# Optimization experiments

Hardware: AMD Instinct MI355X
Metric: run time of the kernel (lower is better)

Reference implementation:

```python
import jax, jax.numpy as jnp
import numpy as np

B, T, F = 4096, 60, 30
H, HD, LAT = 256, 100, 256
ACQ_VOCAB = [(50, 16), (10, 8), (5, 4)]
SEQ_VOCAB = [(30, 8), (12, 4), (31, 4)]
DIN = F + 28 + 16  # 74 = seq_n_features + emb_acq_sum + emb_seq_sum
EPS = 1e-5


def setup_inputs() -> dict:
    key = jax.random.key(0)
    ks = iter(jax.random.split(key, 64))

    def nrm(shape, s=0.05):
        return jax.random.normal(next(ks), shape, jnp.float32) * s

    inp = {}
    inp["seq"] = jax.random.normal(next(ks), (B, T, F), jnp.float32)
    inp["seq_len"] = jnp.sort(jax.random.randint(next(ks), (B,), 1, T + 1))[::-1]  # descending (pack_padded)
    inp["ymd"] = jnp.stack([jax.random.randint(next(ks), (B, T), 0, c) for c, _ in SEQ_VOCAB], axis=-1)
    inp["acq"] = jnp.stack([jax.random.randint(next(ks), (B,), 0, c) for c, _ in ACQ_VOCAB], axis=-1)
    inp["macro_pred"] = jax.random.normal(next(ks), (B, 12, 14), jnp.float32)
    inp["z_noise"] = jax.random.normal(next(ks), (B, LAT), jnp.float32)  # reparam noise, fixed for determinism
    for i, (c, d) in enumerate(ACQ_VOCAB):
        inp[f"E_acq{i}"] = nrm((c, d), 1.0)
    for i, (c, d) in enumerate(SEQ_VOCAB):
        inp[f"E_seq{i}"] = nrm((c, d), 1.0)
    for tag in ("f", "b"):  # bidirectional LSTM, 1 layer
        inp[f"Wih_{tag}"] = nrm((4 * H, DIN))
        inp[f"Whh_{tag}"] = nrm((4 * H, H))
        inp[f"bih_{tag}"] = nrm((4 * H,))
        inp[f"bhh_{tag}"] = nrm((4 * H,))
    inp["W_lat"] = nrm((2 * LAT, H)); inp["b_lat"] = nrm((2 * LAT,))
    inp["Wih1"] = nrm((4 * HD, LAT + 9 + 14)); inp["Whh1"] = nrm((4 * HD, HD))
    inp["bih1"] = nrm((4 * HD,)); inp["bhh1"] = nrm((4 * HD,))
    inp["Wih2"] = nrm((4 * HD, HD)); inp["Whh2"] = nrm((4 * HD, HD))
    inp["bih2"] = nrm((4 * HD,)); inp["bhh2"] = nrm((4 * HD,))
    inp["Wg1"] = nrm((25, HD)); inp["bg1"] = nrm((25,))
    inp["gamma"] = jnp.ones((25,), jnp.float32); inp["beta"] = jnp.zeros((25,), jnp.float32)
    inp["Wg2"] = nrm((9, 25)); inp["bg2"] = nrm((9,))
    return inp


def _lstm_cell(x, h, c, Wih, Whh, bih, bhh):
    g = x @ Wih.T + h @ Whh.T + (bih + bhh)
    i, f, gg, o = jnp.split(g, 4, axis=-1)  # torch gate order i,f,g,o
    c = jax.nn.sigmoid(f) * c + jax.nn.sigmoid(i) * jnp.tanh(gg)
    h = jax.nn.sigmoid(o) * jnp.tanh(c)
    return h, c


def _masked_lstm(xs_tm, lens, Wih, Whh, bih, bhh):
    """xs_tm: [T,B,D] time-major. Returns hidden at each sequence's final valid step."""
    h0 = jnp.zeros((xs_tm.shape[1], Whh.shape[1]), xs_tm.dtype)

    def step(carry, inp):
        h, c = carry
        x, t = inp
        hn, cn = _lstm_cell(x, h, c, Wih, Whh, bih, bhh)
        m = (t < lens)[:, None]
        return (jnp.where(m, hn, h), jnp.where(m, cn, c)), None

    (h, _), _ = jax.lax.scan(step, (h0, h0), (xs_tm, jnp.arange(xs_tm.shape[0])))
    return h


def reference(seq, seq_len, ymd, acq, macro_pred, z_noise,
              E_acq0, E_acq1, E_acq2, E_seq0, E_seq1, E_seq2,
              Wih_f, Whh_f, bih_f, bhh_f, Wih_b, Whh_b, bih_b, bhh_b,
              W_lat, b_lat, Wih1, Whh1, bih1, bhh1, Wih2, Whh2, bih2, bhh2,
              Wg1, bg1, gamma, beta, Wg2, bg2):
    Bn, Tn = seq.shape[0], seq.shape[1]
    ea = jnp.concatenate([E_acq0[acq[:, 0]], E_acq1[acq[:, 1]], E_acq2[acq[:, 2]]], axis=1)
    ea = jnp.broadcast_to(ea[:, None, :], (Bn, Tn, ea.shape[1]))
    ey = jnp.concatenate([E_seq0[ymd[:, :, 0]], E_seq1[ymd[:, :, 1]], E_seq2[ymd[:, :, 2]]], axis=2)
    s = jnp.concatenate([seq, ea, ey], axis=2)  # [B,T,74]

    # bidirectional LSTM over valid lengths (pack_padded semantics)
    h_f = _masked_lstm(jnp.swapaxes(s, 0, 1), seq_len, Wih_f, Whh_f, bih_f, bhh_f)
    idx = jnp.clip(seq_len[:, None] - 1 - jnp.arange(Tn)[None, :], 0, Tn - 1)  # per-seq reversed valid indices
    s_rev = jnp.take_along_axis(s, idx[:, :, None], axis=1)
    h_b = _masked_lstm(jnp.swapaxes(s_rev, 0, 1), seq_len, Wih_b, Whh_b, bih_b, bhh_b)

    lat = (h_f + h_b) @ W_lat.T + b_lat  # [B, 2*LAT]
    mu_z, logv = lat[:, :LAT], lat[:, LAT:]
    z = mu_z + jnp.sqrt(jnp.exp(logv)) * z_noise

    dlq0 = jnp.take_along_axis(seq, (seq_len - 1)[:, None, None], axis=1)[:, 0, -9:]  # [B,9]
    h0 = jnp.zeros((Bn, HD), seq.dtype)

    def dec_step(carry, mp_t):
        h1, c1, h2, c2, dlq = carry
        decinp = jnp.concatenate([z, dlq, mp_t], axis=1)  # [B, LAT+9+14]
        h1, c1 = _lstm_cell(decinp, h1, c1, Wih1, Whh1, bih1, bhh1)
        h2, c2 = _lstm_cell(h1, h2, c2, Wih2, Whh2, bih2, bhh2)  # dropout = identity (eval)
        x = jax.nn.relu(h2 @ Wg1.T + bg1)
        mu = x.mean(axis=0)
        var = ((x - mu) ** 2).mean(axis=0)  # train-mode BN, biased var
        x = gamma * (x - mu) * jax.lax.rsqrt(var + EPS) + beta
        dlq = x @ Wg2.T + bg2
        return (h1, c1, h2, c2, dlq), dlq

    _, outs = jax.lax.scan(dec_step, (h0, h0, h0, h0, dlq0), jnp.swapaxes(macro_pred, 0, 1))
    return jnp.transpose(outs, (1, 2, 0))  # [B, 9, 12] (torch.stack(out, 2))
```

## Files before the change

kernel.cpp:

```cpp
#include <hip/hip_runtime.h>
#include <math.h>

#define B_SZ   4096
#define T_SZ   60
#define F_SZ   30
#define H_ENC  256
#define HD_DEC 100
#define LATD   256
#define KM     352
#define KMP    360
#define NKK    11
#define DTAIL  24

enum {
  OFF_PWM_F = 0,
  OFF_PWM_B = OFF_PWM_F + 180224,
  OFF_BEN_F = OFF_PWM_B + 180224,
  OFF_BEN_B = OFF_BEN_F + 1024,
  OFF_PLAT  = OFF_BEN_B + 1024,
  OFF_P1I   = OFF_PLAT + 256*256*2,
  OFF_P1H   = OFF_P1I + 280*100*4,
  OFF_P2I   = OFF_P1H + 100*100*4,
  OFF_P2H   = OFF_P2I + 100*100*4,
  OFF_WG1T  = OFF_P2H + 100*100*4,
  OFF_BE1   = OFF_WG1T + 100*25,
  OFF_BE2   = OFF_BE1 + 400,
  OFF_HF    = OFF_BE2 + 400,
  OFF_HB    = OFF_HF + B_SZ*H_ENC,
  OFF_H1    = OFF_HB + B_SZ*H_ENC,
  OFF_C1    = OFF_H1 + B_SZ*HD_DEC,
  OFF_H2    = OFF_C1 + B_SZ*HD_DEC,
  OFF_C2    = OFF_H2 + B_SZ*HD_DEC,
  OFF_DLQ   = OFF_C2 + B_SZ*HD_DEC,
  OFF_XBUF  = OFF_DLQ + B_SZ*9,
  OFF_MU    = OFF_XBUF + B_SZ*25,
  OFF_RSTD  = OFF_MU + 25,
  OFF_ZW1   = OFF_RSTD + 25,
  WS_FLOATS = OFF_ZW1 + B_SZ*400
};

typedef __attribute__((ext_vector_type(8))) short short8v;
typedef __attribute__((ext_vector_type(4))) float f32x4;

__device__ __forceinline__ float sigf(float x) { return 1.0f / (1.0f + expf(-x)); }

__device__ __forceinline__ unsigned short f2bf(float f) {
  union { float f; unsigned int u; } v; v.f = f;
  unsigned int u = v.u + 0x7fffu + ((v.u >> 16) & 1u);
  return (unsigned short)(u >> 16);
}
__device__ __forceinline__ float bf2f(unsigned short s) {
  union { unsigned int u; float f; } v; v.u = ((unsigned int)s) << 16;
  return v.f;
}

struct PJob { const float* a; const float* b; float* dst; int p0, p1, p2, p3, mode; };
struct PrepArgs { PJob j[12]; };

__device__ __forceinline__ float enc_wv(const float* wih, const float* whh, int k, int u, int g) {
  if (k < 74)  return wih[(g * 256 + u) * 74 + k];
  if (k < 76)  return 0.0f;
  if (k < 332) return whh[(g * 256 + u) * 256 + (k - 76)];
  return 0.0f;
}

__global__ __launch_bounds__(256) void prep_kernel(PrepArgs pa) {
  int gtid = blockIdx.x * blockDim.x + threadIdx.x;
  int stride = gridDim.x * blockDim.x;
  for (int jj = 0; jj < 12; ++jj) {
    PJob jb = pa.j[jj];
    if (jb.mode == 1) {
      for (int i = gtid; i < jb.p0; i += stride) jb.dst[i] = jb.a[i] + jb.b[i];
    } else if (jb.mode == 0) {
      int total = jb.p2 * jb.p0;
      for (int i = gtid; i < total; i += stride) {
        int k = i / jb.p0, u = i - k * jb.p0;
        float* d = jb.dst + (size_t)i * jb.p3;
        for (int g = 0; g < jb.p3; ++g)
          d[g] = (k < jb.p1) ? jb.a[(g * jb.p0 + u) * jb.p1 + k] : 0.0f;
      }
    } else if (jb.mode == 4) {
      int total = NKK * 64 * 64;
      for (int i = gtid; i < total; i += stride) {
        int kk = i / 4096, rem = i - kk * 4096;
        int ntg = rem >> 6, l = rem & 63;
        int n = ntg * 16 + (l & 15);
        int u = n >> 2, g = n & 3;
        int kb = kk * 32 + (l >> 4) * 8;
        unsigned int* d = (unsigned int*)jb.dst + (size_t)i * 4;
        for (int wd = 0; wd < 4; ++wd) {
          float lo = enc_wv(jb.a, jb.b, kb + 2 * wd,     u, g);
          float hi = enc_wv(jb.a, jb.b, kb + 2 * wd + 1, u, g);
          d[wd] = (unsigned int)f2bf(lo) | ((unsigned int)f2bf(hi) << 16);
        }
      }
    } else {
      for (int i = gtid; i < 1024; i += stride) {
        int u = i >> 2, g = i & 3;
        jb.dst[i] = jb.a[g * 256 + u] + jb.b[g * 256 + u];
      }
    }
  }
}

#define GDOT(acc, c, w0, w1, w2, w3, xv) \
  acc = fmaf((w0).c, (xv).x, fmaf((w1).c, (xv).y, fmaf((w2).c, (xv).z, fmaf((w3).c, (xv).w, acc))))

__global__ __launch_bounds__(512) void enc_kernel(
    const float* __restrict__ seq, const int* __restrict__ seq_len,
    const int* __restrict__ ymd, const int* __restrict__ acq,
    const float* __restrict__ Ea0, const float* __restrict__ Ea1, const float* __restrict__ Ea2,
    const float* __restrict__ Es0, const float* __restrict__ Es1, const float* __restrict__ Es2,
    const unsigned short* __restrict__ PWMf, const unsigned short* __restrict__ PWMb,
    const float* __restrict__ benF, const float* __restrict__ benB,
    float* __restrict__ hf_out, float* __restrict__ hb_out)
{
  const int tid = threadIdx.x;
  const bool bwd = blockIdx.x >= 128;
  const int c = blockIdx.x & 127;
  const unsigned short* __restrict__ PWM = bwd ? PWMb : PWMf;
  const float* __restrict__ ben = bwd ? benB : benF;
  float* __restrict__ hout = bwd ? hb_out : hf_out;

  __shared__ __align__(16) unsigned short v_s[32][KMP];
  __shared__ float c_s[32][256];
  __shared__ int   len_s[32];

  for (int i = tid; i < 32 * KMP; i += 512) (&v_s[0][0])[i] = 0;
  for (int i = tid; i < 32 * 256; i += 512) (&c_s[0][0])[i] = 0.0f;
  if (tid < 32) len_s[tid] = seq_len[c + 128 * tid];
  __syncthreads();

  for (int i = tid; i < 32 * 28; i += 512) {
    int r = i / 28, d = i - r * 28;
    const int* aq = &acq[(c + 128 * r) * 3];
    float v;
    if (d < 16)      v = Ea0[aq[0] * 16 + d];
    else if (d < 24) v = Ea1[aq[1] * 8 + (d - 16)];
    else             v = Ea2[aq[2] * 4 + (d - 24)];
    v_s[r][30 + d] = f2bf(v);
  }

  const int w   = tid >> 6;
  const int l   = tid & 63;
  const int col = l & 15;
  const int qk  = l >> 4;
  const int g   = l & 3;
  const int usub = col >> 2;

  float bias_r[8];
  #pragma unroll
  for (int nt = 0; nt < 8; ++nt) bias_r[nt] = ben[128 * w + 16 * nt + col];

  __syncthreads();
  const int maxlen = len_s[0];

  for (int t = 0; t < maxlen; ++t) {
    for (int i = tid; i < 1472; i += 512) {
      if (i < 960) {
        int r = i / 30, k = i - r * 30;
        int len = len_s[r];
        int te = bwd ? max(len - 1 - t, 0) : t;
        v_s[r][k] = f2bf(seq[((size_t)(c + 128 * r) * T_SZ + te) * F_SZ + k]);
      } else {
        int ii = i - 960;
        int r = ii >> 4, d = ii & 15;
        int len = len_s[r];
        int te = bwd ? max(len - 1 - t, 0) : t;
        const int* ym = &ymd[((size_t)(c + 128 * r) * T_SZ + te) * 3];
        float v;
        if (d < 8)       v = Es0[ym[0] * 8 + d];
        else if (d < 12) v = Es1[ym[1] * 4 + (d - 8)];
        else             v = Es2[ym[2] * 4 + (d - 12)];
        v_s[r][58 + d] = f2bf(v);
      }
    }
    __syncthreads();

    f32x4 acc0[8], acc1[8];
    #pragma unroll
    for (int nt = 0; nt < 8; ++nt) {
      acc0[nt][0] = bias_r[nt]; acc0[nt][1] = bias_r[nt];
      acc0[nt][2] = bias_r[nt]; acc0[nt][3] = bias_r[nt];
      acc1[nt] = acc0[nt];
    }

    for (int kk = 0; kk < NKK; ++kk) {
      short8v a0 = *reinterpret_cast<const short8v*>(&v_s[col][32 * kk + 8 * qk]);
      short8v a1 = *reinterpret_cast<const short8v*>(&v_s[16 + col][32 * kk + 8 * qk]);
      const unsigned short* Bk = PWM + ((size_t)kk * 4096 + l) * 8;
      #pragma unroll
      for (int nt = 0; nt < 8; ++nt) {
        int ntg = 8 * w + nt;
        short8v b = *reinterpret_cast<const short8v*>(Bk + (size_t)ntg * 512);
        acc0[nt] = __builtin_amdgcn_mfma_f32_16x16x32_bf16(a0, b, acc0[nt], 0, 0, 0);
        acc1[nt] = __builtin_amdgcn_mfma_f32_16x16x32_bf16(a1, b, acc1[nt], 0, 0, 0);
      }
    }
    __syncthreads();

    #pragma unroll
    for (int rt = 0; rt < 2; ++rt) {
      #pragma unroll
      for (int nt = 0; nt < 8; ++nt) {
        int u = 32 * w + 4 * nt + usub;
        #pragma unroll
        for (int i = 0; i < 4; ++i) {
          int row = 16 * rt + qk * 4 + i;
          float val = rt == 0 ? acc0[nt][i] : acc1[nt][i];
          float act = (g == 2) ? tanhf(val) : sigf(val);
          float a1s = __shfl_xor(act, 1);
          float a2s = __shfl_xor(act, 2);
          float a3s = __shfl_xor(a1s, 2);
          if (g == 0 && t < len_s[row]) {
            float cc = c_s[row][u];
            float cn = a1s * cc + act * a2s;
            c_s[row][u] = cn;
            v_s[row][76 + u] = f2bf(a3s * tanhf(cn));
          }
        }
      }
    }
  }

  __syncthreads();
  for (int i = tid; i < 32 * 256; i += 512) {
    int r = i >> 8, u = i & 255;
    hout[(size_t)(c + 128 * r) * H_ENC + u] = bf2f(v_s[r][76 + u]);
  }
}

__global__ __launch_bounds__(256) void latent_kernel(
    const float* __restrict__ hf, const float* __restrict__ hb,
    const float2* __restrict__ Plat, const float* __restrict__ b_lat,
    const float* __restrict__ z_noise, const float* __restrict__ seq,
    const int* __restrict__ seq_len, const float4* __restrict__ P1I,
    float* __restrict__ dlq, float* __restrict__ zw1,
    float* __restrict__ h1w, float* __restrict__ c1w,
    float* __restrict__ h2w, float* __restrict__ c2w)
{
  const int tid = threadIdx.x;
  const int b0 = blockIdx.x * 16;
  __shared__ float hs[16][H_ENC];
  for (int i = tid; i < 16 * H_ENC; i += 256)
    (&hs[0][0])[i] = hf[b0 * H_ENC + i] + hb[b0 * H_ENC + i];
  __syncthreads();

  const int u = tid;
  const float bm = b_lat[u], bv = b_lat[LATD + u];
  float am[16], av[16];
  #pragma unroll
  for (int r = 0; r < 16; ++r) { am[r] = bm; av[r] = bv; }

  for (int k = 0; k < H_ENC; k += 4) {
    const float2 p0 = Plat[(k + 0) * 256 + u];
    const float2 p1 = Plat[(k + 1) * 256 + u];
    const float2 p2 = Plat[(k + 2) * 256 + u];
    const float2 p3 = Plat[(k + 3) * 256 + u];
    #pragma unroll
    for (int r = 0; r < 16; ++r) {
      const float4 hv = *reinterpret_cast<const float4*>(&hs[r][k]);
      am[r] = fmaf(p0.x, hv.x, fmaf(p1.x, hv.y, fmaf(p2.x, hv.z, fmaf(p3.x, hv.w, am[r]))));
      av[r] = fmaf(p0.y, hv.x, fmaf(p1.y, hv.y, fmaf(p2.y, hv.z, fmaf(p3.y, hv.w, av[r]))));
    }
  }
  if (u < HD_DEC) {
    #pragma unroll
    for (int r = 0; r < 16; ++r) {
      int b = b0 + r;
      h1w[b * HD_DEC + u] = 0.0f; c1w[b * HD_DEC + u] = 0.0f;
      h2w[b * HD_DEC + u] = 0.0f; c2w[b * HD_DEC + u] = 0.0f;
    }
  }
  if (u < 9) {
    #pragma unroll
    for (int r = 0; r < 16; ++r) {
      int b = b0 + r;
      int len = seq_len[b];
      dlq[b * 9 + u] = seq[(b * T_SZ + (len - 1)) * F_SZ + 21 + u];
    }
  }
  __syncthreads();
  #pragma unroll
  for (int r = 0; r < 16; ++r) {
    int b = b0 + r;
    hs[r][u] = am[r] + sqrtf(expf(av[r])) * z_noise[b * LATD + u];
  }
  __syncthreads();

  const int uu = tid & 127;
  const int grp = tid >> 7;
  const int r0 = grp * 8;
  if (uu < HD_DEC) {
    float a0[8], a1[8], a2[8], a3[8];
    #pragma unroll
    for (int r = 0; r < 8; ++r) { a0[r] = 0.0f; a1[r] = 0.0f; a2[r] = 0.0f; a3[r] = 0.0f; }
    for (int k = 0; k < LATD; k += 4) {
      const float4 w0 = P1I[(k + 0) * 100 + uu];
      const float4 w1 = P1I[(k + 1) * 100 + uu];
      const float4 w2 = P1I[(k + 2) * 100 + uu];
      const float4 w3 = P1I[(k + 3) * 100 + uu];
      #pragma unroll
      for (int r = 0; r < 8; ++r) {
        const float4 xv = *reinterpret_cast<const float4*>(&hs[r0 + r][k]);
        GDOT(a0[r], x, w0, w1, w2, w3, xv);
        GDOT(a1[r], y, w0, w1, w2, w3, xv);
        GDOT(a2[r], z, w0, w1, w2, w3, xv);
        GDOT(a3[r], w, w0, w1, w2, w3, xv);
      }
    }
    #pragma unroll
    for (int r = 0; r < 8; ++r) {
      int b = b0 + r0 + r;
      zw1[b * 400 + uu]       = a0[r];
      zw1[b * 400 + 100 + uu] = a1[r];
      zw1[b * 400 + 200 + uu] = a2[r];
      zw1[b * 400 + 300 + uu] = a3[r];
    }
  }
}

__global__ __launch_bounds__(256) void dec_cell_kernel(
    const float* __restrict__ zw1, const float* __restrict__ dlq0,
    const float* __restrict__ macro,
    float* __restrict__ h1w, float* __restrict__ c1w,
    float* __restrict__ h2w, float* __restrict__ c2w,
    const float4* __restrict__ P1I, const float4* __restrict__ P1H, const float* __restrict__ be1,
    const float4* __restrict__ P2I, const float4* __restrict__ P2H, const float* __restrict__ be2,
    const float* __restrict__ Wg1T, const float* __restrict__ bg1,
    const float* __restrict__ muv, const float* __restrict__ rstdv,
    const float* __restrict__ gamma, const float* __restrict__ beta,
    const float* __restrict__ Wg2, const float* __restrict__ bg2,
    float* __restrict__ xbuf, float* __restrict__ out, int t)
{
  const int tid = threadIdx.x;
  const int b0 = blockIdx.x * 16;
  __shared__ float di[16][DTAIL];
  __shared__ float xns[16][25];
  __shared__ float h1s[16][HD_DEC];
  __shared__ float h2s[16][HD_DEC];

  if (t > 0) {
    for (int p = tid; p < 16 * 25; p += 256) {
      int r = p / 25, cc = p - r * 25;
      xns[r][cc] = gamma[cc] * (xbuf[(b0 + r) * 25 + cc] - muv[cc]) * rstdv[cc] + beta[cc];
    }
  } else {
    for (int p = tid; p < 16 * 9; p += 256) {
      int r = p / 9, j = p - r * 9;
      di[r][j] = dlq0[(b0 + r) * 9 + j];
    }
  }
  for (int i = tid; i < 16 * 15; i += 256) {
    int r = i / 15, k = i - r * 15;
    di[r][9 + k] = (k < 14) ? macro[((size_t)(b0 + r) * 12 + t) * 14 + k] : 0.0f;
  }
  for (int i = tid; i < 16 * HD_DEC; i += 256) {
    int r = i / HD_DEC, k = i - r * HD_DEC;
    h1s[r][k] = h1w[(b0 + r) * HD_DEC + k];
    h2s[r][k] = h2w[(b0 + r) * HD_DEC + k];
  }
  __syncthreads();
  if (t > 0) {
    for (int p = tid; p < 16 * 9; p += 256) {
      int r = p / 9, j = p - r * 9;
      float s = bg2[j];
      #pragma unroll
      for (int cc = 0; cc < 25; ++cc) s += xns[r][cc] * Wg2[j * 25 + cc];
      di[r][j] = s;
      out[(size_t)(b0 + r) * 108 + j * 12 + (t - 1)] = s;
    }
  }

  const int u = tid & 127;
  const int grp = tid >> 7;
  const int r0 = grp * 8;
  const bool act = u < HD_DEC;

  float c1r[8], c2r[8];
  if (act) {
    #pragma unroll
    for (int r = 0; r < 8; ++r) {
      c1r[r] = c1w[(b0 + r0 + r) * HD_DEC + u];
      c2r[r] = c2w[(b0 + r0 + r) * HD_DEC + u];
    }
  }
  __syncthreads();

  float a0[8], a1[8], a2[8], a3[8];
  if (act) {
    const float b0g = be1[u], b1g = be1[100 + u], b2g = be1[200 + u], b3g = be1[300 + u];
    #pragma unroll
    for (int r = 0; r < 8; ++r) {
      const float* zw = &zw1[(size_t)(b0 + r0 + r) * 400];
      a0[r] = b0g + zw[u];
      a1[r] = b1g + zw[100 + u];
      a2[r] = b2g + zw[200 + u];
      a3[r] = b3g + zw[300 + u];
    }
    for (int k = 0; k < DTAIL; k += 4) {
      const int kk = LATD + k;
      const float4 w0 = P1I[(kk + 0) * 100 + u];
      const float4 w1 = P1I[(kk + 1) * 100 + u];
      const float4 w2 = P1I[(kk + 2) * 100 + u];
      const float4 w3 = P1I[(kk + 3) * 100 + u];
      #pragma unroll
      for (int r = 0; r < 8; ++r) {
        const float4 xv = *reinterpret_cast<const float4*>(&di[r0 + r][k]);
        GDOT(a0[r], x, w0, w1, w2, w3, xv);
        GDOT(a1[r], y, w0, w1, w2, w3, xv);
        GDOT(a2[r], z, w0, w1, w2, w3, xv);
        GDOT(a3[r], w, w0, w1, w2, w3, xv);
      }
    }
    for (int k = 0; k < HD_DEC; k += 4) {
      const float4 w0 = P1H[(k + 0) * 100 + u];
      const float4 w1 = P1H[(k + 1) * 100 + u];
      const float4 w2 = P1H[(k + 2) * 100 + u];
      const float4 w3 = P1H[(k + 3) * 100 + u];
      #pragma unroll
      for (int r = 0; r < 8; ++r) {
        const float4 hv = *reinterpret_cast<const float4*>(&h1s[r0 + r][k]);
        GDOT(a0[r], x, w0, w1, w2, w3, hv);
        GDOT(a1[r], y, w0, w1, w2, w3, hv);
        GDOT(a2[r], z, w0, w1, w2, w3, hv);
        GDOT(a3[r], w, w0, w1, w2, w3, hv);
      }
    }
  }
  __syncthreads();
  if (act) {
    #pragma unroll
    for (int r = 0; r < 8; ++r) {
      float ig = sigf(a0[r]), fg = sigf(a1[r]), gg = tanhf(a2[r]), og = sigf(a3[r]);
      float cn = fg * c1r[r] + ig * gg;
      float hn = og * tanhf(cn);
      int b = b0 + r0 + r;
      h1s[r0 + r][u] = hn;
      h1w[b * HD_DEC + u] = hn;
      c1w[b * HD_DEC + u] = cn;
    }
  }
  __syncthreads();

  if (act) {
    const float b0g = be2[u], b1g = be2[100 + u], b2g = be2[200 + u], b3g = be2[300 + u];
    #pragma unroll
    for (int r = 0; r < 8; ++r) { a0[r] = b0g; a1[r] = b1g; a2[r] = b2g; a3[r] = b3g; }
    for (int k = 0; k < HD_DEC; k += 4) {
      const float4 w0 = P2I[(k + 0) * 100 + u];
      const float4 w1 = P2I[(k + 1) * 100 + u];
      const float4 w2 = P2I[(k + 2) * 100 + u];
      const float4 w3 = P2I[(k + 3) * 100 + u];
      #pragma unroll
      for (int r = 0; r < 8; ++r) {
        const float4 hv = *reinterpret_cast<const float4*>(&h1s[r0 + r][k]);
        GDOT(a0[r], x, w0, w1, w2, w3, hv);
        GDOT(a1[r], y, w0, w1, w2, w3, hv);
        GDOT(a2[r], z, w0, w1, w2, w3, hv);
        GDOT(a3[r], w, w0, w1, w2, w3, hv);
      }
    }
    for (int k = 0; k < HD_DEC; k += 4) {
      const float4 w0 = P2H[(k + 0) * 100 + u];
      const float4 w1 = P2H[(k + 1) * 100 + u];
      const float4 w2 = P2H[(k + 2) * 100 + u];
      const float4 w3 = P2H[(k + 3) * 100 + u];
      #pragma unroll
      for (int r = 0; r < 8; ++r) {
        const float4 hv = *reinterpret_cast<const float4*>(&h2s[r0 + r][k]);
        GDOT(a0[r], x, w0, w1, w2, w3, hv);
        GDOT(a1[r], y, w0, w1, w2, w3, hv);
        GDOT(a2[r], z, w0, w1, w2, w3, hv);
        GDOT(a3[r], w, w0, w1, w2, w3, hv);
      }
    }
  }
  __syncthreads();
  if (act) {
    #pragma unroll
    for (int r = 0; r < 8; ++r) {
      float ig = sigf(a0[r]), fg = sigf(a1[r]), gg = tanhf(a2[r]), og = sigf(a3[r]);
      float cn = fg * c2r[r] + ig * gg;
      float hn = og * tanhf(cn);
      int b = b0 + r0 + r;
      h2s[r0 + r][u] = hn;
      h2w[b * HD_DEC + u] = hn;
      c2w[b * HD_DEC + u] = cn;
    }
  }
  __syncthreads();

  for (int p = tid; p < 16 * 25; p += 256) {
    int r = p / 25, cc = p - r * 25;
    float s = bg1[cc];
    for (int k = 0; k < HD_DEC; k += 4) {
      const float4 hv = *reinterpret_cast<const float4*>(&h2s[r][k]);
      s += hv.x * Wg1T[k * 25 + cc] + hv.y * Wg1T[(k + 1) * 25 + cc]
         + hv.z * Wg1T[(k + 2) * 25 + cc] + hv.w * Wg1T[(k + 3) * 25 + cc];
    }
    xbuf[(b0 + r) * 25 + cc] = fmaxf(s, 0.0f);
  }
}

__global__ __launch_bounds__(256) void dec_stats_kernel(
    const float* __restrict__ xbuf, float* __restrict__ muv, float* __restrict__ rstdv)
{
  const int col = blockIdx.x;
  const int tid = threadIdx.x;
  __shared__ float red[256];
  float v[16];
  float s = 0.0f;
  #pragma unroll
  for (int i = 0; i < 16; ++i) { v[i] = xbuf[(tid + 256 * i) * 25 + col]; s += v[i]; }
  red[tid] = s; __syncthreads();
  for (int off = 128; off >= 1; off >>= 1) {
    if (tid < off) red[tid] += red[tid + off];
    __syncthreads();
  }
  float mean = red[0] / (float)B_SZ;
  __syncthreads();
  float s2 = 0.0f;
  #pragma unroll
  for (int i = 0; i < 16; ++i) { float d = v[i] - mean; s2 += d * d; }
  red[tid] = s2; __syncthreads();
  for (int off = 128; off >= 1; off >>= 1) {
    if (tid < off) red[tid] += red[tid + off];
    __syncthreads();
  }
  if (tid == 0) {
    muv[col] = mean;
    rstdv[col] = rsqrtf(red[0] / (float)B_SZ + 1e-5f);
  }
}

__global__ __launch_bounds__(256) void dec_finalout_kernel(
    const float* __restrict__ xbuf, const float* __restrict__ muv, const float* __restrict__ rstdv,
    const float* __restrict__ gamma, const float* __restrict__ beta,
    const float* __restrict__ Wg2, const float* __restrict__ bg2,
    float* __restrict__ out)
{
  int b = blockIdx.x * 256 + threadIdx.x;
  float xn[25];
  #pragma unroll
  for (int c = 0; c < 25; ++c)
    xn[c] = gamma[c] * (xbuf[b * 25 + c] - muv[c]) * rstdv[c] + beta[c];
  #pragma unroll
  for (int j = 0; j < 9; ++j) {
    float s = bg2[j];
    #pragma unroll
    for (int c = 0; c < 25; ++c) s += xn[c] * Wg2[j * 25 + c];
    out[(size_t)b * 108 + j * 12 + 11] = s;
  }
}

extern "C" void kernel_launch(void* const* d_in, const int* in_sizes, int n_in,
                              void* d_out, int out_size, void* d_ws, size_t ws_size,
                              hipStream_t stream)
{
  const float* seq     = (const float*)d_in[0];
  const int*   seq_len = (const int*)  d_in[1];
  const int*   ymd     = (const int*)  d_in[2];
  const int*   acq     = (const int*)  d_in[3];
  const float* macro   = (const float*)d_in[4];
  const float* z_noise = (const float*)d_in[5];
  const float* Ea0 = (const float*)d_in[6];
  const float* Ea1 = (const float*)d_in[7];
  const float* Ea2 = (const float*)d_in[8];
  const float* Es0 = (const float*)d_in[9];
  const float* Es1 = (const float*)d_in[10];
  const float* Es2 = (const float*)d_in[11];
  const float* Wih_f = (const float*)d_in[12];
  const float* Whh_f = (const float*)d_in[13];
  const float* bih_f = (const float*)d_in[14];
  const float* bhh_f = (const float*)d_in[15];
  const float* Wih_b = (const float*)d_in[16];
  const float* Whh_b = (const float*)d_in[17];
  const float* bih_b = (const float*)d_in[18];
  const float* bhh_b = (const float*)d_in[19];
  const float* W_lat = (const float*)d_in[20];
  const float* b_lat = (const float*)d_in[21];
  const float* Wih1  = (const float*)d_in[22];
  const float* Whh1  = (const float*)d_in[23];
  const float* bih1  = (const float*)d_in[24];
  const float* bhh1  = (const float*)d_in[25];
  const float* Wih2  = (const float*)d_in[26];
  const float* Whh2  = (const float*)d_in[27];
  const float* bih2  = (const float*)d_in[28];
  const float* bhh2  = (const float*)d_in[29];
  const float* Wg1   = (const float*)d_in[30];
  const float* bg1   = (const float*)d_in[31];
  const float* gamma = (const float*)d_in[32];
  const float* beta  = (const float*)d_in[33];
  const float* Wg2   = (const float*)d_in[34];
  const float* bg2   = (const float*)d_in[35];

  float* ws  = (float*)d_ws;
  float* out = (float*)d_out;

  float* pwmF = ws + OFF_PWM_F;
  float* pwmB = ws + OFF_PWM_B;
  float* benF = ws + OFF_BEN_F;
  float* benB = ws + OFF_BEN_B;
  float* plat = ws + OFF_PLAT;
  float* p1i  = ws + OFF_P1I;
  float* p1h  = ws + OFF_P1H;
  float* p2i  = ws + OFF_P2I;
  float* p2h  = ws + OFF_P2H;
  float* wg1T = ws + OFF_WG1T;
  float* be1  = ws + OFF_BE1;
  float* be2  = ws + OFF_BE2;
  float* hf   = ws + OFF_HF;
  float* hb   = ws + OFF_HB;
  float* h1w  = ws + OFF_H1;
  float* c1w  = ws + OFF_C1;
  float* h2w  = ws + OFF_H2;
  float* c2w  = ws + OFF_C2;
  float* dlq  = ws + OFF_DLQ;
  float* xbuf = ws + OFF_XBUF;
  float* muv  = ws + OFF_MU;
  float* rstdv= ws + OFF_RSTD;
  float* zw1  = ws + OFF_ZW1;

  PrepArgs pa;
  int ji = 0;
  auto JOB = [&](const float* a, const float* b, float* d, int p0, int p1, int p2, int p3, int m) {
    pa.j[ji].a = a; pa.j[ji].b = b; pa.j[ji].dst = d;
    pa.j[ji].p0 = p0; pa.j[ji].p1 = p1; pa.j[ji].p2 = p2; pa.j[ji].p3 = p3; pa.j[ji].mode = m; ++ji;
  };
  JOB(Wih_f, Whh_f, pwmF, 0,0,0,0, 4);
  JOB(Wih_b, Whh_b, pwmB, 0,0,0,0, 4);
  JOB(bih_f, bhh_f, benF, 0,0,0,0, 5);
  JOB(bih_b, bhh_b, benB, 0,0,0,0, 5);
  JOB(W_lat, nullptr, plat, 256, 256, 256, 2, 0);
  JOB(Wih1,  nullptr, p1i,  100, 279, 280, 4, 0);
  JOB(Whh1,  nullptr, p1h,  100, 100, 100, 4, 0);
  JOB(Wih2,  nullptr, p2i,  100, 100, 100, 4, 0);
  JOB(Whh2,  nullptr, p2h,  100, 100, 100, 4, 0);
  JOB(Wg1,   nullptr, wg1T, 25, 100, 100, 1, 0);
  JOB(bih1,  bhh1,  be1,  400, 0,0,0, 1);
  JOB(bih2,  bhh2,  be2,  400, 0,0,0, 1);

  prep_kernel<<<512, 256, 0, stream>>>(pa);

  enc_kernel<<<256, 512, 0, stream>>>(
      seq, seq_len, ymd, acq, Ea0, Ea1, Ea2, Es0, Es1, Es2,
      (const unsigned short*)pwmF, (const unsigned short*)pwmB,
      benF, benB, hf, hb);

  latent_kernel<<<256, 256, 0, stream>>>(
      hf, hb, (const float2*)plat, b_lat, z_noise, seq, seq_len,
      (const float4*)p1i, dlq, zw1, h1w, c1w, h2w, c2w);

  for (int t = 0; t < 12; ++t) {
    dec_cell_kernel<<<256, 256, 0, stream>>>(
        zw1, dlq, macro, h1w, c1w, h2w, c2w,
        (const float4*)p1i, (const float4*)p1h, be1,
        (const float4*)p2i, (const float4*)p2h, be2, wg1T, bg1,
        muv, rstdv, gamma, beta, Wg2, bg2, xbuf, out, t);
    dec_stats_kernel<<<25, 256, 0, stream>>>(xbuf, muv, rstdv);
  }
  dec_finalout_kernel<<<16, 256, 0, stream>>>(
      xbuf, muv, rstdv, gamma, beta, Wg2, bg2, out);
}
```

Baseline: 3.020 ms.

## Process 64 sequences per encoder block to amortize weight streaming

The encoder LSTM block now handles 64 batch rows instead of 32, with grid size halved to 128 blocks. Each wave loads a weight fragment once and reuses it across four row tiles instead of two, which cuts global/L2 weight traffic per sequence. The gate computation is split into two halves of hidden units, and the first half's hidden outputs are staged in a new LDS buffer so the second half still reads the previous hidden state. The cost is that only half as many blocks run (about half the CUs on a 256-CU part), and each step does twice the MFMA and epilogue work per block plus an extra copy pass.

```diff
diff --git a/kernel.cpp b/kernel.cpp
--- a/kernel.cpp
+++ b/kernel.cpp
@@ -116,24 +116,25 @@
     float* __restrict__ hf_out, float* __restrict__ hb_out)
 {
   const int tid = threadIdx.x;
-  const bool bwd = blockIdx.x >= 128;
-  const int c = blockIdx.x & 127;
+  const bool bwd = blockIdx.x >= 64;
+  const int c = blockIdx.x & 63;
   const unsigned short* __restrict__ PWM = bwd ? PWMb : PWMf;
   const float* __restrict__ ben = bwd ? benB : benF;
   float* __restrict__ hout = bwd ? hb_out : hf_out;
 
-  __shared__ __align__(16) unsigned short v_s[32][KMP];
-  __shared__ float c_s[32][256];
-  __shared__ int   len_s[32];
-
-  for (int i = tid; i < 32 * KMP; i += 512) (&v_s[0][0])[i] = 0;
-  for (int i = tid; i < 32 * 256; i += 512) (&c_s[0][0])[i] = 0.0f;
-  if (tid < 32) len_s[tid] = seq_len[c + 128 * tid];
-  __syncthreads();
-
-  for (int i = tid; i < 32 * 28; i += 512) {
+  __shared__ __align__(16) unsigned short v_s[64][KMP];
+  __shared__ __align__(16) unsigned short hnew[64][128];
+  __shared__ float c_s[64][256];
+  __shared__ int   len_s[64];
+
+  for (int i = tid; i < 64 * KMP; i += 512) (&v_s[0][0])[i] = 0;
+  for (int i = tid; i < 64 * 256; i += 512) (&c_s[0][0])[i] = 0.0f;
+  if (tid < 64) len_s[tid] = seq_len[c + 64 * tid];
+  __syncthreads();
+
+  for (int i = tid; i < 64 * 28; i += 512) {
     int r = i / 28, d = i - r * 28;
-    const int* aq = &acq[(c + 128 * r) * 3];
+    const int* aq = &acq[(c + 64 * r) * 3];
     float v;
     if (d < 16)      v = Ea0[aq[0] * 16 + d];
     else if (d < 24) v = Ea1[aq[1] * 8 + (d - 16)];
@@ -148,26 +149,29 @@
   const int g   = l & 3;
   const int usub = col >> 2;
 
-  float bias_r[8];
+  float bias0[4], bias1[4];
   #pragma unroll
-  for (int nt = 0; nt < 8; ++nt) bias_r[nt] = ben[128 * w + 16 * nt + col];
+  for (int nt = 0; nt < 4; ++nt) {
+    bias0[nt] = ben[16 * (4 * w + nt) + col];
+    bias1[nt] = ben[16 * (32 + 4 * w + nt) + col];
+  }
 
   __syncthreads();
   const int maxlen = len_s[0];
 
   for (int t = 0; t < maxlen; ++t) {
-    for (int i = tid; i < 1472; i += 512) {
-      if (i < 960) {
+    for (int i = tid; i < 2944; i += 512) {
+      if (i < 1920) {
         int r = i / 30, k = i - r * 30;
         int len = len_s[r];
         int te = bwd ? max(len - 1 - t, 0) : t;
-        v_s[r][k] = f2bf(seq[((size_t)(c + 128 * r) * T_SZ + te) * F_SZ + k]);
+        v_s[r][k] = f2bf(seq[((size_t)(c + 64 * r) * T_SZ + te) * F_SZ + k]);
       } else {
-        int ii = i - 960;
+        int ii = i - 1920;
         int r = ii >> 4, d = ii & 15;
         int len = len_s[r];
         int te = bwd ? max(len - 1 - t, 0) : t;
-        const int* ym = &ymd[((size_t)(c + 128 * r) * T_SZ + te) * 3];
+        const int* ym = &ymd[((size_t)(c + 64 * r) * T_SZ + te) * 3];
         float v;
         if (d < 8)       v = Es0[ym[0] * 8 + d];
         else if (d < 12) v = Es1[ym[1] * 4 + (d - 8)];
@@ -177,56 +181,113 @@
     }
     __syncthreads();
 
-    f32x4 acc0[8], acc1[8];
-    #pragma unroll
-    for (int nt = 0; nt < 8; ++nt) {
-      acc0[nt][0] = bias_r[nt]; acc0[nt][1] = bias_r[nt];
-      acc0[nt][2] = bias_r[nt]; acc0[nt][3] = bias_r[nt];
-      acc1[nt] = acc0[nt];
-    }
-
-    for (int kk = 0; kk < NKK; ++kk) {
-      short8v a0 = *reinterpret_cast<const short8v*>(&v_s[col][32 * kk + 8 * qk]);
-      short8v a1 = *reinterpret_cast<const short8v*>(&v_s[16 + col][32 * kk + 8 * qk]);
-      const unsigned short* Bk = PWM + ((size_t)kk * 4096 + l) * 8;
-      #pragma unroll
-      for (int nt = 0; nt < 8; ++nt) {
-        int ntg = 8 * w + nt;
-        short8v b = *reinterpret_cast<const short8v*>(Bk + (size_t)ntg * 512);
-        acc0[nt] = __builtin_amdgcn_mfma_f32_16x16x32_bf16(a0, b, acc0[nt], 0, 0, 0);
-        acc1[nt] = __builtin_amdgcn_mfma_f32_16x16x32_bf16(a1, b, acc1[nt], 0, 0, 0);
-      }
-    }
-    __syncthreads();
-
-    #pragma unroll
-    for (int rt = 0; rt < 2; ++rt) {
-      #pragma unroll
-      for (int nt = 0; nt < 8; ++nt) {
-        int u = 32 * w + 4 * nt + usub;
+    {
+      f32x4 acc[4][4];
+      #pragma unroll
+      for (int rt = 0; rt < 4; ++rt)
         #pragma unroll
-        for (int i = 0; i < 4; ++i) {
-          int row = 16 * rt + qk * 4 + i;
-          float val = rt == 0 ? acc0[nt][i] : acc1[nt][i];
-          float act = (g == 2) ? tanhf(val) : sigf(val);
-          float a1s = __shfl_xor(act, 1);
-          float a2s = __shfl_xor(act, 2);
-          float a3s = __shfl_xor(a1s, 2);
-          if (g == 0 && t < len_s[row]) {
-            float cc = c_s[row][u];
-            float cn = a1s * cc + act * a2s;
-            c_s[row][u] = cn;
-            v_s[row][76 + u] = f2bf(a3s * tanhf(cn));
+        for (int nt = 0; nt < 4; ++nt) {
+          acc[rt][nt][0] = bias0[nt]; acc[rt][nt][1] = bias0[nt];
+          acc[rt][nt][2] = bias0[nt]; acc[rt][nt][3] = bias0[nt];
+        }
+      for (int kk = 0; kk < NKK; ++kk) {
+        short8v a[4];
+        #pragma unroll
+        for (int rt = 0; rt < 4; ++rt)
+          a[rt] = *reinterpret_cast<const short8v*>(&v_s[16 * rt + col][32 * kk + 8 * qk]);
+        const unsigned short* Bk = PWM + ((size_t)kk * 4096 + l) * 8;
+        #pragma unroll
+        for (int nt = 0; nt < 4; ++nt) {
+          int ntg = 4 * w + nt;
+          short8v b = *reinterpret_cast<const short8v*>(Bk + (size_t)ntg * 512);
+          #pragma unroll
+          for (int rt = 0; rt < 4; ++rt)
+            acc[rt][nt] = __builtin_amdgcn_mfma_f32_16x16x32_bf16(a[rt], b, acc[rt][nt], 0, 0, 0);
+        }
+      }
+      #pragma unroll
+      for (int rt = 0; rt < 4; ++rt) {
+        #pragma unroll
+        for (int nt = 0; nt < 4; ++nt) {
+          int u = 16 * w + 4 * nt + usub;
+          #pragma unroll
+          for (int i = 0; i < 4; ++i) {
+            int row = 16 * rt + qk * 4 + i;
+            float val = acc[rt][nt][i];
+            float act = (g == 2) ? tanhf(val) : sigf(val);
+            float a1s = __shfl_xor(act, 1);
+            float a2s = __shfl_xor(act, 2);
+            float a3s = __shfl_xor(a1s, 2);
+            if (g == 0 && t < len_s[row]) {
+              float cc = c_s[row][u];
+              float cn = a1s * cc + act * a2s;
+              c_s[row][u] = cn;
+              hnew[row][u] = f2bf(a3s * tanhf(cn));
+            }
           }
         }
       }
     }
-  }
-
-  __syncthreads();
-  for (int i = tid; i < 32 * 256; i += 512) {
+
+    {
+      f32x4 acc[4][4];
+      #pragma unroll
+      for (int rt = 0; rt < 4; ++rt)
+        #pragma unroll
+        for (int nt = 0; nt < 4; ++nt) {
+          acc[rt][nt][0] = bias1[nt]; acc[rt][nt][1] = bias1[nt];
+          acc[rt][nt][2] = bias1[nt]; acc[rt][nt][3] = bias1[nt];
+        }
+      for (int kk = 0; kk < NKK; ++kk) {
+        short8v a[4];
+        #pragma unroll
+        for (int rt = 0; rt < 4; ++rt)
+          a[rt] = *reinterpret_cast<const short8v*>(&v_s[16 * rt + col][32 * kk + 8 * qk]);
+        const unsigned short* Bk = PWM + ((size_t)kk * 4096 + l) * 8;
+        #pragma unroll
+        for (int nt = 0; nt < 4; ++nt) {
+          int ntg = 32 + 4 * w + nt;
+          short8v b = *reinterpret_cast<const short8v*>(Bk + (size_t)ntg * 512);
+          #pragma unroll
+          for (int rt = 0; rt < 4; ++rt)
+            acc[rt][nt] = __builtin_amdgcn_mfma_f32_16x16x32_bf16(a[rt], b, acc[rt][nt], 0, 0, 0);
+        }
+      }
+      __syncthreads();
+      #pragma unroll
+      for (int rt = 0; rt < 4; ++rt) {
+        #pragma unroll
+        for (int nt = 0; nt < 4; ++nt) {
+          int u = 128 + 16 * w + 4 * nt + usub;
+          #pragma unroll
+          for (int i = 0; i < 4; ++i) {
+            int row = 16 * rt + qk * 4 + i;
+            float val = acc[rt][nt][i];
+            float act = (g == 2) ? tanhf(val) : sigf(val);
+            float a1s = __shfl_xor(act, 1);
+            float a2s = __shfl_xor(act, 2);
+            float a3s = __shfl_xor(a1s, 2);
+            if (g == 0 && t < len_s[row]) {
+              float cc = c_s[row][u];
+              float cn = a1s * cc + act * a2s;
+              c_s[row][u] = cn;
+              v_s[row][76 + u] = f2bf(a3s * tanhf(cn));
+            }
+          }
+        }
+      }
+    }
+
+    for (int i = tid; i < 64 * 128; i += 512) {
+      int row = i >> 7, u = i & 127;
+      if (t < len_s[row]) v_s[row][76 + u] = hnew[row][u];
+    }
+  }
+
+  __syncthreads();
+  for (int i = tid; i < 64 * 256; i += 512) {
     int r = i >> 8, u = i & 255;
-    hout[(size_t)(c + 128 * r) * H_ENC + u] = bf2f(v_s[r][76 + u]);
+    hout[(size_t)(c + 64 * r) * H_ENC + u] = bf2f(v_s[r][76 + u]);
   }
 }
 
@@ -643,7 +704,7 @@
 
   prep_kernel<<<512, 256, 0, stream>>>(pa);
 
-  enc_kernel<<<256, 512, 0, stream>>>(
+  enc_kernel<<<128, 512, 0, stream>>>(
       seq, seq_len, ymd, acq, Ea0, Ea1, Ea2, Es0, Es1, Es2,
       (const unsigned short*)pwmF, (const unsigned short*)pwmB,
       benF, benB, hf, hb);
```

Measured after the change: 4.445 ms. 47.2% more time.
